# Optimization experiments

Hardware: AMD Instinct MI355X
Metric: run time of the kernel (lower is better)

## Reference

```python
import jax, jax.numpy as jnp
import numpy as np

CUTOFF = 5.0
EPS = 1e-3  # keras BatchNormalization default epsilon
L = 3       # num_interactions
N = 100000
E = 1600000
H = 64
FIN = 16


def setup_inputs() -> dict:
    key = jax.random.key(0)
    ks = jax.random.split(key, 16)
    s = 0.1  # weight scale for numerical stability
    return {
        "x": jax.random.normal(ks[0], (N, FIN), jnp.float32),
        "edge_index": jax.random.randint(ks[1], (2, E), 0, N, jnp.int32),
        "distances": jax.random.uniform(ks[2], (E,), jnp.float32) * CUTOFF,
        "edge_attr": jax.random.normal(ks[3], (E, 1), jnp.float32),
        "emb_W": jax.random.normal(ks[4], (FIN, H), jnp.float32) * s,
        "emb_b": jnp.zeros((H,), jnp.float32),
        "fW1": jax.random.normal(ks[5], (L, 1, H), jnp.float32) * s,
        "fb1": jnp.zeros((L, H), jnp.float32),
        "fW2": jax.random.normal(ks[6], (L, H, H), jnp.float32) * s,
        "fb2": jnp.zeros((L, H), jnp.float32),
        "iW1": jax.random.normal(ks[7], (L, H, H), jnp.float32) * s,
        "ib1": jnp.zeros((L, H), jnp.float32),
        "iW2": jax.random.normal(ks[8], (L, H, H), jnp.float32) * s,
        "ib2": jnp.zeros((L, H), jnp.float32),
        "bn_gamma": jnp.ones((L, H), jnp.float32),
        "bn_beta": jnp.zeros((L, H), jnp.float32),
        "oW1": jax.random.normal(ks[9], (H, H // 2), jnp.float32) * s,
        "ob1": jnp.zeros((H // 2,), jnp.float32),
        "og1": jnp.ones((H // 2,), jnp.float32),
        "obt1": jnp.zeros((H // 2,), jnp.float32),
        "oW2": jax.random.normal(ks[10], (H // 2, H // 2), jnp.float32) * s,
        "ob2": jnp.zeros((H // 2,), jnp.float32),
        "og2": jnp.ones((H // 2,), jnp.float32),
        "obt2": jnp.zeros((H // 2,), jnp.float32),
        "fin_W": jax.random.normal(ks[11], (H // 2, 3), jnp.float32) * s,
        "fin_b": jnp.zeros((3,), jnp.float32),
    }


def reference(x, edge_index, distances, edge_attr,
              emb_W, emb_b, fW1, fb1, fW2, fb2,
              iW1, ib1, iW2, ib2, bn_gamma, bn_beta,
              oW1, ob1, og1, obt1, oW2, ob2, og2, obt2,
              fin_W, fin_b):
    n_nodes = x.shape[0]
    row, col = edge_index[0], edge_index[1]
    inv = 1.0 / jnp.sqrt(1.0 + EPS)  # BN inference with moving mean=0, var=1

    # shared edge-level quantities
    scaled = distances * (2.0 / CUTOFF) - 1.0                       # [E]
    cut = 0.5 * (jnp.cos(distances * np.pi / CUTOFF) + 1.0)
    cut = jnp.where(distances <= CUTOFF, cut, 0.0)                  # [E]

    h = x @ emb_W + emb_b                                           # [N,H]
    for l in range(L):
        # filter MLP: [E,1] -> [E,F]
        f = jnp.tanh(scaled[:, None] * fW1[l][0] + fb1[l]) @ fW2[l] + fb2[l]
        f = f * cut[:, None]
        # original: sum_F(neighbor[:,None,:] * f[:,:,None]) == neighbor * sum_F(f)
        fs = f.sum(-1)                                              # [E]
        msgs = h[col] * fs[:, None]                                 # [E,H] gather
        agg = jax.ops.segment_sum(msgs, row, num_segments=n_nodes)  # [N,H] scatter-add
        out = jax.nn.softplus(agg @ iW1[l] + ib1[l]) @ iW2[l] + ib2[l]
        out = out * inv * bn_gamma[l] + bn_beta[l]                  # BN (inference)
        h = h + out

    g = h.mean(axis=0)                                              # [H]
    g = jax.nn.softplus(g @ oW1 + ob1) * inv * og1 + obt1
    g = jax.nn.softplus(g @ oW2 + ob2) * inv * og2 + obt2
    return g @ fin_W + fin_b                                        # [3]
```

## Files before the change

kernel.cpp:

```cpp
#include <hip/hip_runtime.h>
#include <hip/hip_fp16.h>
#include <math.h>

#define CUTOFF 5.0f
#define H 64
#define FIN 16
#define NLAYERS 3
#define LUTN 2048
#define LUTSTRIDE 2052
#define ASTRIDE 72
#define MEANB 256
#define BROWS 512
#define NBMAX 256
#define MAXC 10240
#define ABLK 4096

#define BN_INV 0.999500374750f

typedef _Float16 h8 __attribute__((ext_vector_type(8)));
typedef _Float16 h2 __attribute__((ext_vector_type(2)));
typedef float f32x4 __attribute__((ext_vector_type(4)));
typedef unsigned int u32x2 __attribute__((ext_vector_type(2)));

__device__ __forceinline__ float softplus_f(float x) {
    return fmaxf(x, 0.f) + __logf(1.f + __expf(-fabsf(x)));
}

__global__ __launch_bounds__(1024)
void k_pre(const float* __restrict__ x, const float* __restrict__ emb_W,
           const float* __restrict__ emb_b, _Float16* __restrict__ h0,
           const float* __restrict__ fW1, const float* __restrict__ fb1,
           const float* __restrict__ fW2, const float* __restrict__ fb2,
           const float* __restrict__ iW1, const float* __restrict__ iW2,
           const float* __restrict__ bn_g, const float* __restrict__ bn_b,
           const float* __restrict__ ib2, h8* __restrict__ Wsw,
           float* __restrict__ b2p, float* __restrict__ lut,
           const int* __restrict__ ei, const float* __restrict__ dist,
           unsigned int* __restrict__ cursor, u32x2* __restrict__ stg,
           int N, int E, int NB, int nbA, int nbE16) {
    __shared__ u32x2 s_rec[ABLK];
    __shared__ unsigned s_cnt[NBMAX];
    __shared__ unsigned s_x[NBMAX];
    __shared__ unsigned s_ofs[NBMAX];
    __shared__ unsigned s_gbase[NBMAX];
    __shared__ float swsum[64];
    __shared__ float sbsum;
    int b = blockIdx.x;
    int t = threadIdx.x;
    if (b < nbA) {
        int e0 = b * ABLK;
        int nE = min(ABLK, E - e0);
        for (int i = t; i < NBMAX; i += 1024) s_cnt[i] = 0;
        __syncthreads();
        int rowv[4];
        unsigned rxv[4] = {0u, 0u, 0u, 0u};
#pragma unroll
        for (int j = 0; j < 4; j++) {
            int li = j * 1024 + t;
            rowv[j] = -1;
            if (li < nE) {
                int e = e0 + li;
                int r = ei[e];
                int col = ei[E + e];
                float d = dist[e];
                int didx = (int)(d * (32768.0f / CUTOFF) + 0.5f);
                didx = max(0, min(didx, 32767));
                rowv[j] = r;
                rxv[j] = ((unsigned)col << 15) | (unsigned)didx;
                atomicAdd(&s_cnt[r / BROWS], 1u);
            }
        }
        __syncthreads();
        if (t < NBMAX) s_x[t] = s_cnt[t];
        __syncthreads();
        for (int off = 1; off < NBMAX; off <<= 1) {
            unsigned v = 0;
            if (t < NBMAX && t >= off) v = s_x[t - off];
            __syncthreads();
            if (t < NBMAX) s_x[t] += v;
            __syncthreads();
        }
        if (t < NBMAX) {
            unsigned c = s_cnt[t];
            unsigned lstart = s_x[t] - c;
            s_ofs[t] = lstart;
            s_x[t] = lstart;
            s_gbase[t] = (c && t < (unsigned)NB) ? atomicAdd(&cursor[t], c) : 0u;
        }
        __syncthreads();
#pragma unroll
        for (int j = 0; j < 4; j++) {
            if (rowv[j] >= 0) {
                unsigned slot = atomicAdd(&s_ofs[rowv[j] / BROWS], 1u);
                u32x2 rec;
                rec.x = rxv[j];
                rec.y = (unsigned)rowv[j];
                s_rec[slot] = rec;
            }
        }
        __syncthreads();
        for (int i = t; i < nE; i += 1024) {
            u32x2 rec = s_rec[i];
            int bk = (int)(rec.y / BROWS);
            unsigned g = s_gbase[bk] + ((unsigned)i - s_x[bk]);
            if (g < MAXC)
                stg[(size_t)bk * MAXC + g] = rec;
        }
    } else if (b < nbA + nbE16) {
        int lane = t & 63;
        int w = t >> 6;
        int node = (b - nbA) * 16 + w;
        if (node < N) {
            float acc = emb_b[lane];
#pragma unroll
            for (int k = 0; k < FIN; k++) acc += x[node * FIN + k] * emb_W[k * H + lane];
            h0[(size_t)node * H + lane] = (_Float16)acc;
        }
    } else if (b < nbA + nbE16 + NLAYERS * 3) {
        int lb = b - nbA - nbE16;
        int l = lb / 3, part = lb % 3;
        if (t < 64) {
            float s = 0.f;
            for (int j = 0; j < H; j++) s += fW2[l * H * H + t * H + j];
            swsum[t] = s;
        }
        if (t == 64) {
            float s = 0.f;
            for (int j = 0; j < H; j++) s += fb2[l * H + j];
            sbsum = s;
        }
        __syncthreads();
        int i = part * 1024 + t;
        if (i <= LUTN) {
            float d = (float)i * (CUTOFF / (float)LUTN);
            float scaled = d * (2.0f / CUTOFF) - 1.0f;
            float cut = 0.5f * (__cosf(d * (3.14159265358979f / CUTOFF)) + 1.0f);
            if (d > CUTOFF) cut = 0.f;
            float s = 0.f;
            for (int hh = 0; hh < H; hh++) {
                int wi = l * H + hh;
                s += tanhf(scaled * fW1[wi] + fb1[wi]) * swsum[hh];
            }
            lut[l * LUTSTRIDE + i] = cut * (s + sbsum);
        }
    } else {
        int tid = (b - nbA - nbE16 - NLAYERS * 3) * 1024 + t;
        if (tid < NLAYERS * H)
            b2p[tid] = ib2[tid] * BN_INV * bn_g[tid] + bn_b[tid];
        if (tid < NLAYERS * 2 * 8 * 64) {
            int lane = tid & 63;
            int frag = (tid >> 6) & 7;
            int mat  = (tid >> 9) & 1;
            int l    = tid >> 10;
            int kt = frag >> 2, nt = frag & 3;
            int n = nt * 16 + (lane & 15);
            int k0 = kt * 32 + (lane >> 4) * 8;
            const float* W = (mat ? iW2 : iW1) + l * H * H;
            float scale = mat ? BN_INV * bn_g[l * H + n] : 1.0f;
            h8 v;
#pragma unroll
            for (int j = 0; j < 8; j++) v[j] = (_Float16)(W[(k0 + j) * H + n] * scale);
            Wsw[tid] = v;
        }
    }
}

__global__ __launch_bounds__(1024)
void k_passB(const u32x2* __restrict__ stg, const unsigned int* __restrict__ cursor,
             int* __restrict__ row_ptr, unsigned int* __restrict__ recs,
             int N, int NB) {
    __shared__ int s_bb[NBMAX];
    __shared__ int s_c[BROWS];
    __shared__ int s_x[BROWS];
    __shared__ unsigned s_out[MAXC];
    int b = blockIdx.x, t = threadIdx.x;
    if (t < NBMAX) {
        int cb = 0;
        if (t < NB) cb = min((int)cursor[t], MAXC);
        s_bb[t] = cb;
    }
    __syncthreads();
    for (int off = 1; off < NBMAX; off <<= 1) {
        int v = 0;
        if (t < NBMAX && t >= off) v = s_bb[t - off];
        __syncthreads();
        if (t < NBMAX) s_bb[t] += v;
        __syncthreads();
    }
    int bbase = (b > 0) ? s_bb[b - 1] : 0;
    int cnt = s_bb[b] - bbase;
    int r0 = b * BROWS;
    int r1 = min(r0 + BROWS, N);
    int nrows = r1 - r0;
    const u32x2* mystg = stg + (size_t)b * MAXC;
    u32x2 myrec[10];
    int nmine = 0;
#pragma unroll
    for (int i = 0; i < 10; i++) {
        int idx = t + i * 1024;
        if (idx < cnt) { myrec[i] = mystg[idx]; nmine = i + 1; }
    }
    if (t < BROWS) s_c[t] = 0;
    __syncthreads();
#pragma unroll
    for (int i = 0; i < 10; i++)
        if (i < nmine) atomicAdd(&s_c[(int)myrec[i].y - r0], 1);
    __syncthreads();
    if (t < BROWS) s_x[t] = s_c[t];
    __syncthreads();
    for (int off = 1; off < BROWS; off <<= 1) {
        int v = 0;
        if (t < BROWS && t >= off) v = s_x[t - off];
        __syncthreads();
        if (t < BROWS) s_x[t] += v;
        __syncthreads();
    }
    if (t < nrows) {
        int excl = s_x[t] - s_c[t];
        row_ptr[r0 + t] = bbase + excl;
        s_c[t] = excl;
    }
    if (b == NB - 1 && t == 0) row_ptr[N] = bbase + cnt;
    __syncthreads();
#pragma unroll
    for (int i = 0; i < 10; i++)
        if (i < nmine) {
            int slot = atomicAdd(&s_c[(int)myrec[i].y - r0], 1);
            s_out[slot] = myrec[i].x;
        }
    __syncthreads();
    for (int i = t; i < cnt; i += 1024)
        recs[bbase + i] = s_out[i];
}

#define PROC4(KK, SS, TT, ACC) do {                                          \
    int _lim = ((TT) > (SS)) ? (TT) - 1 : 0;                                 \
    int _ka = min((KK), _lim),     _kb = min((KK) + 1, _lim);                \
    int _kc = min((KK) + 2, _lim), _kd = min((KK) + 3, _lim);                \
    unsigned _ra = recs[_ka], _rb = recs[_kb];                               \
    unsigned _rc = recs[_kc], _rd = recs[_kd];                               \
    float _ta = (float)(_ra & 32767u) * (1.0f / 16.0f);                      \
    float _tb = (float)(_rb & 32767u) * (1.0f / 16.0f);                      \
    float _tc = (float)(_rc & 32767u) * (1.0f / 16.0f);                      \
    float _td = (float)(_rd & 32767u) * (1.0f / 16.0f);                      \
    int _ia = (int)_ta, _ib = (int)_tb, _ic = (int)_tc, _id = (int)_td;      \
    float _fa = s_lut[_ia], _fb = s_lut[_ib];                                \
    float _fc = s_lut[_ic], _fd = s_lut[_id];                                \
    float _va = _fa + (_ta - (float)_ia) * (s_lut[_ia + 1] - _fa);           \
    float _vb = _fb + (_tb - (float)_ib) * (s_lut[_ib + 1] - _fb);           \
    float _vc = _fc + (_tc - (float)_ic) * (s_lut[_ic + 1] - _fc);           \
    float _vd = _fd + (_td - (float)_id) * (s_lut[_id + 1] - _fd);           \
    _va = ((KK)     < (TT)) ? _va : 0.f;                                     \
    _vb = ((KK) + 1 < (TT)) ? _vb : 0.f;                                     \
    _vc = ((KK) + 2 < (TT)) ? _vc : 0.f;                                     \
    _vd = ((KK) + 3 < (TT)) ? _vd : 0.f;                                     \
    union { uint4 u; h2 v[4]; } _pa, _pb, _pc, _pd;                          \
    _pa.u = h4[(_ra >> 15) * 8u + (unsigned)ci];                             \
    _pb.u = h4[(_rb >> 15) * 8u + (unsigned)ci];                             \
    _pc.u = h4[(_rc >> 15) * 8u + (unsigned)ci];                             \
    _pd.u = h4[(_rd >> 15) * 8u + (unsigned)ci];                             \
    _Float16 _ha = (_Float16)_va, _hb = (_Float16)_vb;                       \
    _Float16 _hc = (_Float16)_vc, _hd = (_Float16)_vd;                       \
    h2 _aa = (h2){_ha, _ha}, _ab = (h2){_hb, _hb};                           \
    h2 _ac = (h2){_hc, _hc}, _ad = (h2){_hd, _hd};                           \
    _Pragma("unroll")                                                        \
    for (int _q = 0; _q < 4; _q++) (ACC)[_q] += _aa * _pa.v[_q];             \
    _Pragma("unroll")                                                        \
    for (int _q = 0; _q < 4; _q++) (ACC)[_q] += _ab * _pb.v[_q];             \
    _Pragma("unroll")                                                        \
    for (int _q = 0; _q < 4; _q++) (ACC)[_q] += _ac * _pc.v[_q];             \
    _Pragma("unroll")                                                        \
    for (int _q = 0; _q < 4; _q++) (ACC)[_q] += _ad * _pd.v[_q];             \
} while (0)

__global__ __launch_bounds__(256, 6)
void k_layer(const int* __restrict__ row_ptr, const unsigned int* __restrict__ recs,
             const float* __restrict__ lutl, const h8* __restrict__ Wsw,
             const float* __restrict__ b1, const float* __restrict__ b2p,
             const _Float16* __restrict__ h_in, _Float16* __restrict__ h_out,
             float* __restrict__ pA, int N, int last) {
    __shared__ float s_lut[LUTN + 1];
    __shared__ _Float16 sA[64 * ASTRIDE];
    for (int i = threadIdx.x; i <= LUTN; i += 256) s_lut[i] = lutl[i];
    __syncthreads();

    int lane = threadIdx.x & 63;
    int w = threadIdx.x >> 6;
    int base = blockIdx.x * 64 + w * 16;
    int g = lane >> 3, ci = lane & 7;
    const uint4* h4 = (const uint4*)h_in;

    {
        int node0 = base + g;
        int node1 = base + 8 + g;
        h2 acc0[4], acc1[4];
#pragma unroll
        for (int q = 0; q < 4; q++) {
            acc0[q] = (h2){(_Float16)0.f, (_Float16)0.f};
            acc1[q] = (h2){(_Float16)0.f, (_Float16)0.f};
        }
        int s0 = 0, t0 = 0, s1 = 0, t1 = 0;
        if (node0 < N) { s0 = row_ptr[node0]; t0 = row_ptr[node0 + 1]; }
        if (node1 < N) { s1 = row_ptr[node1]; t1 = row_ptr[node1 + 1]; }
        int it0 = (t0 - s0 + 3) >> 2;
        int it1 = (t1 - s1 + 3) >> 2;
        int iters = max(it0, it1);
        for (int it = 0; it < iters; ++it) {
            int k0 = s0 + it * 4;
            int k1 = s1 + it * 4;
            PROC4(k0, s0, t0, acc0);
            PROC4(k1, s1, t1, acc1);
        }
        union { uint4 u4; h2 v[4]; } pk;
#pragma unroll
        for (int q = 0; q < 4; q++) pk.v[q] = acc0[q];
        *(uint4*)&sA[(size_t)(w * 16 + g) * ASTRIDE + ci * 8] = pk.u4;
#pragma unroll
        for (int q = 0; q < 4; q++) pk.v[q] = acc1[q];
        *(uint4*)&sA[(size_t)(w * 16 + 8 + g) * ASTRIDE + ci * 8] = pk.u4;
    }

    int q4 = lane >> 4, c16 = lane & 15;
    int rowb = w * 16;
    const h8* WB1 = Wsw;
    const h8* WB2 = Wsw + 8 * 64;
    h8 A0 = *(const h8*)&sA[(size_t)(rowb + c16) * ASTRIDE + q4 * 8];
    h8 A1 = *(const h8*)&sA[(size_t)(rowb + c16) * ASTRIDE + 32 + q4 * 8];
    f32x4 C1[4];
#pragma unroll
    for (int nt = 0; nt < 4; nt++) {
        f32x4 c = {0.f, 0.f, 0.f, 0.f};
        c = __builtin_amdgcn_mfma_f32_16x16x32_f16(A0, WB1[nt * 64 + lane], c, 0, 0, 0);
        c = __builtin_amdgcn_mfma_f32_16x16x32_f16(A1, WB1[(4 + nt) * 64 + lane], c, 0, 0, 0);
        C1[nt] = c;
    }
#pragma unroll
    for (int nt = 0; nt < 4; nt++) {
        float bb = b1[nt * 16 + c16];
#pragma unroll
        for (int reg = 0; reg < 4; reg++) {
            float v = softplus_f(C1[nt][reg] + bb);
            sA[(size_t)(rowb + q4 * 4 + reg) * ASTRIDE + nt * 16 + c16] = (_Float16)v;
        }
    }
    h8 M0 = *(const h8*)&sA[(size_t)(rowb + c16) * ASTRIDE + q4 * 8];
    h8 M1 = *(const h8*)&sA[(size_t)(rowb + c16) * ASTRIDE + 32 + q4 * 8];
    f32x4 C2[4];
#pragma unroll
    for (int nt = 0; nt < 4; nt++) {
        f32x4 c = {0.f, 0.f, 0.f, 0.f};
        c = __builtin_amdgcn_mfma_f32_16x16x32_f16(M0, WB2[nt * 64 + lane], c, 0, 0, 0);
        c = __builtin_amdgcn_mfma_f32_16x16x32_f16(M1, WB2[(4 + nt) * 64 + lane], c, 0, 0, 0);
        C2[nt] = c;
    }
    if (!last) {
#pragma unroll
        for (int nt = 0; nt < 4; nt++) {
            float bb2 = b2p[nt * 16 + c16];
#pragma unroll
            for (int reg = 0; reg < 4; reg++) {
                int node = base + q4 * 4 + reg;
                if (node < N) {
                    size_t idx = (size_t)node * H + nt * 16 + c16;
                    float hn = (float)h_in[idx] + C2[nt][reg] + bb2;
                    h_out[idx] = (_Float16)hn;
                }
            }
        }
    } else {
        float ps[4];
#pragma unroll
        for (int nt = 0; nt < 4; nt++) {
            float bb2 = b2p[nt * 16 + c16];
            float s = 0.f;
#pragma unroll
            for (int reg = 0; reg < 4; reg++) {
                int node = base + q4 * 4 + reg;
                if (node < N) {
                    size_t idx = (size_t)node * H + nt * 16 + c16;
                    s += (float)h_in[idx] + C2[nt][reg] + bb2;
                }
            }
            ps[nt] = s;
        }
#pragma unroll
        for (int nt = 0; nt < 4; nt++) {
            float v = ps[nt];
            v += __shfl_xor(v, 16, 64);
            v += __shfl_xor(v, 32, 64);
            if (lane < 16)
                pA[((size_t)blockIdx.x * 4 + w) * H + nt * 16 + c16] = v;
        }
    }
}

__global__ __launch_bounds__(256)
void k_mean(const float* __restrict__ pA, float* __restrict__ partials, int P) {
    __shared__ float s_r[4][H];
    int lane = threadIdx.x & 63;
    int w = threadIdx.x >> 6;
    int wg = blockIdx.x * 4 + w;
    int stride = gridDim.x * 4;
    float local = 0.f;
    for (int i = wg; i < P; i += stride) local += pA[(size_t)i * H + lane];
    s_r[w][lane] = local;
    __syncthreads();
    if (w == 0) {
        float s = s_r[0][lane] + s_r[1][lane] + s_r[2][lane] + s_r[3][lane];
        partials[(size_t)blockIdx.x * H + lane] = s;
    }
}

__global__ __launch_bounds__(256)
void k_final(const float* __restrict__ partials, int N,
             const float* __restrict__ oW1, const float* __restrict__ ob1,
             const float* __restrict__ og1, const float* __restrict__ obt1,
             const float* __restrict__ oW2, const float* __restrict__ ob2,
             const float* __restrict__ og2, const float* __restrict__ obt2,
             const float* __restrict__ fin_W, const float* __restrict__ fin_b,
             float* __restrict__ out) {
    __shared__ float red[4][H];
    __shared__ float sg[H], su[H / 2], sv[H / 2];
    int t = threadIdx.x;
    int ch = t & 63, grp = t >> 6;
    float s = 0.f;
    for (int b = grp; b < MEANB; b += 4) s += partials[(size_t)b * H + ch];
    red[grp][ch] = s;
    __syncthreads();
    if (t < H) sg[t] = (red[0][t] + red[1][t] + red[2][t] + red[3][t]) / (float)N;
    __syncthreads();
    int j = t;
    if (j < H / 2) {
        float acc = ob1[j];
        for (int k = 0; k < H; k++) acc += sg[k] * oW1[k * (H / 2) + j];
        su[j] = softplus_f(acc) * BN_INV * og1[j] + obt1[j];
    }
    __syncthreads();
    if (j < H / 2) {
        float acc = ob2[j];
        for (int k = 0; k < H / 2; k++) acc += su[k] * oW2[k * (H / 2) + j];
        sv[j] = softplus_f(acc) * BN_INV * og2[j] + obt2[j];
    }
    __syncthreads();
    if (j < 3) {
        float acc = fin_b[j];
        for (int k = 0; k < H / 2; k++) acc += sv[k] * fin_W[k * 3 + j];
        out[j] = acc;
    }
}

extern "C" void kernel_launch(void* const* d_in, const int* in_sizes, int n_in,
                              void* d_out, int out_size, void* d_ws, size_t ws_size,
                              hipStream_t stream) {
    const float* x      = (const float*)d_in[0];
    const int*   ei     = (const int*)d_in[1];
    const float* dist   = (const float*)d_in[2];
    const float* emb_W  = (const float*)d_in[4];
    const float* emb_b  = (const float*)d_in[5];
    const float* fW1    = (const float*)d_in[6];
    const float* fb1    = (const float*)d_in[7];
    const float* fW2    = (const float*)d_in[8];
    const float* fb2    = (const float*)d_in[9];
    const float* iW1    = (const float*)d_in[10];
    const float* ib1    = (const float*)d_in[11];
    const float* iW2    = (const float*)d_in[12];
    const float* ib2    = (const float*)d_in[13];
    const float* bn_g   = (const float*)d_in[14];
    const float* bn_b   = (const float*)d_in[15];
    const float* oW1    = (const float*)d_in[16];
    const float* ob1    = (const float*)d_in[17];
    const float* og1    = (const float*)d_in[18];
    const float* obt1   = (const float*)d_in[19];
    const float* oW2    = (const float*)d_in[20];
    const float* ob2    = (const float*)d_in[21];
    const float* og2    = (const float*)d_in[22];
    const float* obt2   = (const float*)d_in[23];
    const float* fin_W  = (const float*)d_in[24];
    const float* fin_b  = (const float*)d_in[25];
    float* out = (float*)d_out;

    int N = in_sizes[0] / FIN;
    int E = in_sizes[2];
    int NB = (N + BROWS - 1) / BROWS;
    int nb_tile = (N + 63) / 64;
    int P = nb_tile * 4;

    float*  ws   = (float*)d_ws;
    _Float16* h0 = (_Float16*)ws;
    _Float16* h1 = h0 + (size_t)N * H;
    unsigned int* recs = (unsigned int*)(h1 + (size_t)N * H);
    h8*     Wsw  = (h8*)(recs + E);
    float*  lut  = (float*)(Wsw + NLAYERS * 2 * 8 * 64);
    float*  partials = lut + 3 * LUTSTRIDE;
    float*  b2p  = partials + MEANB * H;
    float*  pA   = b2p + NLAYERS * H;
    u32x2*  stg  = (u32x2*)(pA + (size_t)P * H);
    int*    row_ptr = (int*)(stg + (size_t)NBMAX * MAXC);
    unsigned int* cursor = (unsigned int*)(row_ptr + N + 1);

    hipMemsetAsync(cursor, 0, NBMAX * sizeof(unsigned int), stream);

    int nbA = (E + ABLK - 1) / ABLK;
    int nbE16 = (N + 15) / 16;
    int nb_pre = nbA + nbE16 + NLAYERS * 3 + 3;
    k_pre<<<nb_pre, 1024, 0, stream>>>(x, emb_W, emb_b, h0,
                                       fW1, fb1, fW2, fb2, iW1, iW2,
                                       bn_g, bn_b, ib2, Wsw, b2p, lut,
                                       ei, dist, cursor, stg,
                                       N, E, NB, nbA, nbE16);

    k_passB<<<NB, 1024, 0, stream>>>(stg, cursor, row_ptr, recs, N, NB);

    _Float16* hp[2] = {h0, h1};
    for (int l = 0; l < NLAYERS; l++) {
        k_layer<<<nb_tile, 256, 0, stream>>>(row_ptr, recs, lut + (size_t)l * LUTSTRIDE,
                                             Wsw + (size_t)l * 1024,
                                             ib1 + l * H, b2p + l * H,
                                             hp[l & 1], hp[(l + 1) & 1], pA, N,
                                             (l == NLAYERS - 1) ? 1 : 0);
    }

    k_mean<<<MEANB, 256, 0, stream>>>(pA, partials, P);
    k_final<<<1, 256, 0, stream>>>(partials, N, oW1, ob1, og1, obt1,
                                   oW2, ob2, og2, obt2, fin_W, fin_b, out);
}
```

Measured before the change: 325.6 us.

## Replicate shared-memory bucket counters and halve row-bucket size in CSR build

The edge binning in k_pre and the per-bucket CSR build in k_passB now keep four replicated counters per bucket, one per 256-thread group. This cuts LDS atomic contention, and the rank returned by the first atomic is reused to compute slots, so the second atomic pass is gone. The bucket size drops from 512 to 256 rows, which gives twice as many passB blocks with half the staging capacity each. The risk is overflow of the smaller MAXC of 5120 for skewed inputs, plus the extra prefix-scan work.

```diff
diff --git a/kernel.cpp b/kernel.cpp
--- a/kernel.cpp
+++ b/kernel.cpp
@@ -10,10 +10,11 @@
 #define LUTSTRIDE 2052
 #define ASTRIDE 72
 #define MEANB 256
-#define BROWS 512
-#define NBMAX 256
-#define MAXC 10240
+#define BROWS 256
+#define NBMAX 512
+#define MAXC 5120
 #define ABLK 4096
+#define NREP 4
 
 #define BN_INV 0.999500374750f
 
@@ -39,9 +40,9 @@
            unsigned int* __restrict__ cursor, u32x2* __restrict__ stg,
            int N, int E, int NB, int nbA, int nbE16) {
     __shared__ u32x2 s_rec[ABLK];
-    __shared__ unsigned s_cnt[NBMAX];
-    __shared__ unsigned s_x[NBMAX];
-    __shared__ unsigned s_ofs[NBMAX];
+    __shared__ unsigned s_cnt[NBMAX * NREP];
+    __shared__ unsigned s_tot[NBMAX];
+    __shared__ unsigned s_gst[NBMAX * NREP];
     __shared__ unsigned s_gbase[NBMAX];
     __shared__ float swsum[64];
     __shared__ float sbsum;
@@ -50,10 +51,12 @@
     if (b < nbA) {
         int e0 = b * ABLK;
         int nE = min(ABLK, E - e0);
-        for (int i = t; i < NBMAX; i += 1024) s_cnt[i] = 0;
+        int gg = t >> 8;
+        for (int i = t; i < NBMAX * NREP; i += 1024) s_cnt[i] = 0;
         __syncthreads();
         int rowv[4];
         unsigned rxv[4] = {0u, 0u, 0u, 0u};
+        unsigned rkv[4] = {0u, 0u, 0u, 0u};
 #pragma unroll
         for (int j = 0; j < 4; j++) {
             int li = j * 1024 + t;
@@ -67,31 +70,41 @@
                 didx = max(0, min(didx, 32767));
                 rowv[j] = r;
                 rxv[j] = ((unsigned)col << 15) | (unsigned)didx;
-                atomicAdd(&s_cnt[r / BROWS], 1u);
+                rkv[j] = atomicAdd(&s_cnt[(r / BROWS) * NREP + gg], 1u);
             }
         }
         __syncthreads();
-        if (t < NBMAX) s_x[t] = s_cnt[t];
+        unsigned tot = 0;
+        if (t < NBMAX) {
+            tot = s_cnt[t * NREP] + s_cnt[t * NREP + 1] +
+                  s_cnt[t * NREP + 2] + s_cnt[t * NREP + 3];
+            s_tot[t] = tot;
+        }
         __syncthreads();
         for (int off = 1; off < NBMAX; off <<= 1) {
             unsigned v = 0;
-            if (t < NBMAX && t >= off) v = s_x[t - off];
+            if (t < NBMAX && t >= off) v = s_tot[t - off];
             __syncthreads();
-            if (t < NBMAX) s_x[t] += v;
+            if (t < NBMAX) s_tot[t] += v;
             __syncthreads();
         }
         if (t < NBMAX) {
-            unsigned c = s_cnt[t];
-            unsigned lstart = s_x[t] - c;
-            s_ofs[t] = lstart;
-            s_x[t] = lstart;
-            s_gbase[t] = (c && t < (unsigned)NB) ? atomicAdd(&cursor[t], c) : 0u;
+            unsigned lstart = s_tot[t] - tot;
+            unsigned runb = lstart;
+#pragma unroll
+            for (int g = 0; g < NREP; g++) {
+                s_gst[t * NREP + g] = runb;
+                runb += s_cnt[t * NREP + g];
+            }
+            s_tot[t] = lstart;
+            s_gbase[t] = (tot && t < (unsigned)NB) ? atomicAdd(&cursor[t], tot) : 0u;
         }
         __syncthreads();
 #pragma unroll
         for (int j = 0; j < 4; j++) {
             if (rowv[j] >= 0) {
-                unsigned slot = atomicAdd(&s_ofs[rowv[j] / BROWS], 1u);
+                int bk = rowv[j] / BROWS;
+                unsigned slot = s_gst[bk * NREP + gg] + rkv[j];
                 u32x2 rec;
                 rec.x = rxv[j];
                 rec.y = (unsigned)rowv[j];
@@ -102,7 +115,7 @@
         for (int i = t; i < nE; i += 1024) {
             u32x2 rec = s_rec[i];
             int bk = (int)(rec.y / BROWS);
-            unsigned g = s_gbase[bk] + ((unsigned)i - s_x[bk]);
+            unsigned g = s_gbase[bk] + ((unsigned)i - s_tot[bk]);
             if (g < MAXC)
                 stg[(size_t)bk * MAXC + g] = rec;
         }
@@ -170,10 +183,12 @@
              int* __restrict__ row_ptr, unsigned int* __restrict__ recs,
              int N, int NB) {
     __shared__ int s_bb[NBMAX];
-    __shared__ int s_c[BROWS];
-    __shared__ int s_x[BROWS];
+    __shared__ unsigned s_c[BROWS * NREP];
+    __shared__ unsigned s_t[BROWS];
+    __shared__ unsigned s_g[BROWS * NREP];
     __shared__ unsigned s_out[MAXC];
     int b = blockIdx.x, t = threadIdx.x;
+    int gg = t >> 8;
     if (t < NBMAX) {
         int cb = 0;
         if (t < NB) cb = min((int)cursor[t], MAXC);
@@ -193,39 +208,51 @@
     int r1 = min(r0 + BROWS, N);
     int nrows = r1 - r0;
     const u32x2* mystg = stg + (size_t)b * MAXC;
-    u32x2 myrec[10];
-    int nmine = 0;
-#pragma unroll
-    for (int i = 0; i < 10; i++) {
+    for (int i = t; i < BROWS * NREP; i += 1024) s_c[i] = 0;
+    __syncthreads();
+    u32x2 myrec[5];
+    unsigned myrk[5] = {0u, 0u, 0u, 0u, 0u};
+    int nm = 0;
+#pragma unroll
+    for (int i = 0; i < 5; i++) {
         int idx = t + i * 1024;
-        if (idx < cnt) { myrec[i] = mystg[idx]; nmine = i + 1; }
-    }
-    if (t < BROWS) s_c[t] = 0;
-    __syncthreads();
-#pragma unroll
-    for (int i = 0; i < 10; i++)
-        if (i < nmine) atomicAdd(&s_c[(int)myrec[i].y - r0], 1);
-    __syncthreads();
-    if (t < BROWS) s_x[t] = s_c[t];
+        if (idx < cnt) {
+            myrec[i] = mystg[idx];
+            myrk[i] = atomicAdd(&s_c[((int)myrec[i].y - r0) * NREP + gg], 1u);
+            nm = i + 1;
+        }
+    }
+    __syncthreads();
+    unsigned tot = 0;
+    if (t < BROWS) {
+        tot = s_c[t * NREP] + s_c[t * NREP + 1] +
+              s_c[t * NREP + 2] + s_c[t * NREP + 3];
+        s_t[t] = tot;
+    }
     __syncthreads();
     for (int off = 1; off < BROWS; off <<= 1) {
-        int v = 0;
-        if (t < BROWS && t >= off) v = s_x[t - off];
-        __syncthreads();
-        if (t < BROWS) s_x[t] += v;
-        __syncthreads();
-    }
-    if (t < nrows) {
-        int excl = s_x[t] - s_c[t];
-        row_ptr[r0 + t] = bbase + excl;
-        s_c[t] = excl;
+        unsigned v = 0;
+        if (t < BROWS && t >= off) v = s_t[t - off];
+        __syncthreads();
+        if (t < BROWS) s_t[t] += v;
+        __syncthreads();
+    }
+    if (t < BROWS) {
+        unsigned excl = s_t[t] - tot;
+        if (t < nrows) row_ptr[r0 + t] = bbase + (int)excl;
+        unsigned runb = excl;
+#pragma unroll
+        for (int g = 0; g < NREP; g++) {
+            s_g[t * NREP + g] = runb;
+            runb += s_c[t * NREP + g];
+        }
     }
     if (b == NB - 1 && t == 0) row_ptr[N] = bbase + cnt;
     __syncthreads();
 #pragma unroll
-    for (int i = 0; i < 10; i++)
-        if (i < nmine) {
-            int slot = atomicAdd(&s_c[(int)myrec[i].y - r0], 1);
+    for (int i = 0; i < 5; i++)
+        if (i < nm) {
+            unsigned slot = s_g[((int)myrec[i].y - r0) * NREP + gg] + myrk[i];
             s_out[slot] = myrec[i].x;
         }
     __syncthreads();
```

New measurement: 323.5 us. About the same (-0.6%).
